# Kernel optimization log

Hardware: AMD Instinct MI355X
Metric: run time of the kernel (lower is better)

The kernel has to match this reference:

```python
import jax, jax.numpy as jnp
import numpy as np

N = 1024
H = 256
EH = max(16, H // 2)  # edge_hidden


def _lin(key, fan_in, fan_out):
    kw, kb = jax.random.split(key)
    s = 1.0 / np.sqrt(fan_in)
    W = jax.random.uniform(kw, (fan_in, fan_out), jnp.float32, -s, s)
    b = jax.random.uniform(kb, (fan_out,), jnp.float32, -s, s)
    return W, b


def setup_inputs() -> dict:
    key = jax.random.key(0)
    ks = jax.random.split(key, 14)
    inp = {
        'h': jax.random.normal(ks[0], (N, H), jnp.float32),
        'delta_local': jax.random.normal(ks[1], (N, 3), jnp.float32),
        't_emb': jax.random.normal(ks[2], (N, 3), jnp.float32),
        'x_current': jax.random.normal(ks[3], (N, 3), jnp.float32),
        'frames': jax.random.normal(ks[4], (N, 3, 3), jnp.float32),
    }
    inp['np1_w'], inp['np1_b'] = _lin(ks[5], H + 6, H)
    inp['np2_w'], inp['np2_b'] = _lin(ks[6], H, H)
    inp['src_w'], inp['src_b'] = _lin(ks[7], H, 1)
    inp['dst_w'], inp['dst_b'] = _lin(ks[8], H, 1)
    inp['ns_w'], inp['ns_b'] = _lin(ks[9], H, 1)
    inp['eg1_w'], inp['eg1_b'] = _lin(ks[10], 4, EH)
    inp['eg2_w'], inp['eg2_b'] = _lin(ks[11], EH, 1)
    inp['out1_w'], inp['out1_b'] = _lin(ks[12], H + 6, H)
    inp['out2_w'], inp['out2_b'] = _lin(ks[13], H, 3)
    return inp


def reference(h, delta_local, t_emb, x_current, frames,
              np1_w, np1_b, np2_w, np2_b,
              src_w, src_b, dst_w, dst_b, ns_w, ns_b,
              eg1_w, eg1_b, eg2_w, eg2_b,
              out1_w, out1_b, out2_w, out2_b):
    silu = jax.nn.silu
    # node_proj: two Linear+SiLU on [h, delta_local, t_emb]
    node_feat = jnp.concatenate([h, delta_local, t_emb], axis=-1)  # [N, H+6]
    node_hidden = silu(silu(node_feat @ np1_w + np1_b) @ np2_w + np2_b)  # [N, H]

    # relative positions in each node's local frame
    rel = x_current[None, :, :] - x_current[:, None, :]             # [N, N, 3], rel[n,m]=x[m]-x[n]
    rel_local = jnp.einsum('nji,nmj->nmi', frames, rel)             # frames^T @ rel
    dist = jnp.linalg.norm(rel_local, axis=-1, keepdims=True)       # [N, N, 1]
    edge_feat = jnp.concatenate([rel_local, dist], axis=-1)         # [N, N, 4]

    # edge-gated attention logits: src + dst + per-edge MLP score
    src = (node_hidden @ src_w + src_b)                             # [N, 1]
    dst = (node_hidden @ dst_w + dst_b)                             # [N, 1]
    edge_logit = silu(edge_feat @ eg1_w + eg1_b) @ eg2_w + eg2_b    # [N, N, 1]
    logits = src[:, None, 0] + dst[None, :, 0] + edge_logit[..., 0] # [N, N]

    eye = jnp.eye(N, dtype=bool)
    logits = jnp.where(eye, -10000.0, logits)
    attn = jax.nn.softmax(logits, axis=1)
    attn = jnp.where(eye, 0.0, attn)
    attn = attn / jnp.maximum(attn.sum(axis=1, keepdims=True), 1e-6)

    ns = jax.nn.sigmoid(node_hidden @ ns_w + ns_b)[:, 0]            # [N]
    local_messages = jnp.einsum('nm,m,nmi->ni', attn, ns, rel_local)  # [N, 3]

    update_feat = jnp.concatenate([node_hidden, delta_local, local_messages], axis=-1)
    local_update = silu(update_feat @ out1_w + out1_b) @ out2_w + out2_b  # [N, 3]
    return local_update + 0.25 * local_messages
```

## Files before the change

kernel.cpp:

```cpp
#include <hip/hip_runtime.h>

#define N 1024
#define H 256
#define EH 128

__device__ __forceinline__ float fast_silu(float x) {
    float u = __builtin_amdgcn_exp2f(x * -1.44269504088896340736f);
    return x * __builtin_amdgcn_rcpf(1.0f + u);
}

__global__ __launch_bounds__(256) void k_node(
    const float* __restrict__ h, const float* __restrict__ dl, const float* __restrict__ temb,
    const float* __restrict__ np1_w, const float* __restrict__ np1_b,
    const float* __restrict__ np2_w, const float* __restrict__ np2_b,
    const float* __restrict__ src_w, const float* __restrict__ src_b,
    const float* __restrict__ dst_w, const float* __restrict__ dst_b,
    const float* __restrict__ ns_w, const float* __restrict__ ns_b,
    const float* __restrict__ eg1_w, const float* __restrict__ eg1_b,
    const float* __restrict__ eg2_w,
    float* __restrict__ nh, float* __restrict__ srcv, float* __restrict__ dstv,
    float* __restrict__ nsv, float* __restrict__ wpA, float* __restrict__ wpB)
{
    const int TILE = 4;
    __shared__ float feat[TILE][264];
    __shared__ float red[TILE][3][4];
    const int tid = threadIdx.x;
    const int blk = blockIdx.x;
    const int n0 = blk * TILE;

    if (blk == 0 && tid < EH) {
        const float NL2E = -1.44269504088896340736f;
        const float NLN2 = -0.69314718055994530942f;
        float4 a;
        a.x = NL2E * eg1_w[0 * EH + tid];
        a.y = NL2E * eg1_w[1 * EH + tid];
        a.z = NL2E * eg1_w[2 * EH + tid];
        a.w = NL2E * eg1_w[3 * EH + tid];
        ((float4*)wpA)[tid] = a;
        float2 b;
        b.x = NL2E * eg1_b[tid];
        b.y = NLN2 * eg2_w[tid];
        ((float2*)wpB)[tid] = b;
    }

    for (int idx = tid; idx < TILE * 264; idx += 256) {
        int t = idx / 264, i = idx % 264;
        int n = n0 + t;
        float v = 0.0f;
        if (i < H)            v = h[n * H + i];
        else if (i < H + 3)   v = dl[n * 3 + (i - H)];
        else if (i < H + 6)   v = temb[n * 3 + (i - H - 3)];
        feat[t][i] = v;
    }
    __syncthreads();

    const int j = tid;
    float acc[TILE];
#pragma unroll
    for (int t = 0; t < TILE; t++) acc[t] = np1_b[j];
    int i = 0;
    for (; i + 4 <= 262; i += 4) {
        float w0 = np1_w[(i + 0) * H + j];
        float w1 = np1_w[(i + 1) * H + j];
        float w2 = np1_w[(i + 2) * H + j];
        float w3 = np1_w[(i + 3) * H + j];
#pragma unroll
        for (int t = 0; t < TILE; t++) {
            float4 f = *(const float4*)&feat[t][i];
            acc[t] = fmaf(f.x, w0, fmaf(f.y, w1, fmaf(f.z, w2, fmaf(f.w, w3, acc[t]))));
        }
    }
    for (; i < 262; i++) {
        float w = np1_w[i * H + j];
#pragma unroll
        for (int t = 0; t < TILE; t++) acc[t] = fmaf(feat[t][i], w, acc[t]);
    }
    __syncthreads();
#pragma unroll
    for (int t = 0; t < TILE; t++) feat[t][j] = fast_silu(acc[t]);
    __syncthreads();

#pragma unroll
    for (int t = 0; t < TILE; t++) acc[t] = np2_b[j];
    for (int i2 = 0; i2 < H; i2 += 4) {
        float w0 = np2_w[(i2 + 0) * H + j];
        float w1 = np2_w[(i2 + 1) * H + j];
        float w2 = np2_w[(i2 + 2) * H + j];
        float w3 = np2_w[(i2 + 3) * H + j];
#pragma unroll
        for (int t = 0; t < TILE; t++) {
            float4 f = *(const float4*)&feat[t][i2];
            acc[t] = fmaf(f.x, w0, fmaf(f.y, w1, fmaf(f.z, w2, fmaf(f.w, w3, acc[t]))));
        }
    }
    float hj[TILE];
#pragma unroll
    for (int t = 0; t < TILE; t++) {
        hj[t] = fast_silu(acc[t]);
        nh[(n0 + t) * H + j] = hj[t];
    }

    float wsc = src_w[j], wdc = dst_w[j], wnc = ns_w[j];
    const int lane = tid & 63, wv = tid >> 6;
#pragma unroll
    for (int t = 0; t < TILE; t++) {
        float ps = hj[t] * wsc, pd = hj[t] * wdc, pn = hj[t] * wnc;
#pragma unroll
        for (int o = 32; o > 0; o >>= 1) {
            ps += __shfl_down(ps, o);
            pd += __shfl_down(pd, o);
            pn += __shfl_down(pn, o);
        }
        if (lane == 0) { red[t][0][wv] = ps; red[t][1][wv] = pd; red[t][2][wv] = pn; }
    }
    __syncthreads();
    if (tid < TILE) {
        int t = tid;
        float s  = red[t][0][0] + red[t][0][1] + red[t][0][2] + red[t][0][3] + src_b[0];
        float d  = red[t][1][0] + red[t][1][1] + red[t][1][2] + red[t][1][3] + dst_b[0];
        float nl = red[t][2][0] + red[t][2][1] + red[t][2][2] + red[t][2][3] + ns_b[0];
        srcv[n0 + t] = s;
        dstv[n0 + t] = d;
        nsv[n0 + t]  = __builtin_amdgcn_rcpf(1.0f + __builtin_amdgcn_exp2f(nl * -1.44269504088896340736f));
    }
}

__global__ __launch_bounds__(256) void k_edge(
    const float* __restrict__ x, const float* __restrict__ frames,
    const float* __restrict__ srcv, const float* __restrict__ dstv,
    const float* __restrict__ nsv,
    const float* __restrict__ wpA, const float* __restrict__ wpB,
    const float* __restrict__ eg2_b, float* __restrict__ msg)
{
    __shared__ float4 WA[EH];
    __shared__ float2 WB[EH];
    __shared__ float rmax[4];
    __shared__ float rsum[4];
    __shared__ float rmsg[3][4];
    const int tid = threadIdx.x;
    const int n = blockIdx.x;

    if (tid < EH) {
        WA[tid] = ((const float4*)wpA)[tid];
        WB[tid] = ((const float2*)wpB)[tid];
    }

    float F[9];
#pragma unroll
    for (int q = 0; q < 9; q++) F[q] = frames[n * 9 + q];
    const float xn0 = x[n * 3 + 0], xn1 = x[n * 3 + 1], xn2 = x[n * 3 + 2];
    const float src_n = srcv[n];
    const float eg2b = eg2_b[0];
    __syncthreads();

    float rl[4][3], dist[4], dstm[4], nsm[4];
#pragma unroll
    for (int e = 0; e < 4; e++) {
        int m = tid + e * 256;
        float rx = x[m * 3 + 0] - xn0;
        float ry = x[m * 3 + 1] - xn1;
        float rz = x[m * 3 + 2] - xn2;
        float r0 = F[0] * rx + F[3] * ry + F[6] * rz;
        float r1 = F[1] * rx + F[4] * ry + F[7] * rz;
        float r2 = F[2] * rx + F[5] * ry + F[8] * rz;
        rl[e][0] = r0; rl[e][1] = r1; rl[e][2] = r2;
        dist[e] = sqrtf(r0 * r0 + r1 * r1 + r2 * r2);
        dstm[e] = dstv[m];
        nsm[e]  = nsv[m];
    }

    float acc[4] = {0.f, 0.f, 0.f, 0.f};
#pragma unroll 4
    for (int k = 0; k < EH; k++) {
        float4 w = WA[k];
        float2 c = WB[k];
#pragma unroll
        for (int e = 0; e < 4; e++) {
            float t2 = fmaf(rl[e][0], w.x, fmaf(rl[e][1], w.y, fmaf(rl[e][2], w.z, fmaf(dist[e], w.w, c.x))));
            float r = __builtin_amdgcn_rcpf(1.0f + __builtin_amdgcn_exp2f(t2));
            acc[e] = fmaf(t2 * r, c.y, acc[e]);
        }
    }

    float lg[4];
#pragma unroll
    for (int e = 0; e < 4; e++) {
        int m = tid + e * 256;
        lg[e] = (m == n) ? -10000.0f : (src_n + dstm[e] + acc[e] + eg2b);
    }

    const int lane = tid & 63, wv = tid >> 6;
    float mx = fmaxf(fmaxf(lg[0], lg[1]), fmaxf(lg[2], lg[3]));
#pragma unroll
    for (int o = 32; o > 0; o >>= 1) mx = fmaxf(mx, __shfl_down(mx, o));
    if (lane == 0) rmax[wv] = mx;
    __syncthreads();
    mx = fmaxf(fmaxf(rmax[0], rmax[1]), fmaxf(rmax[2], rmax[3]));

    float p[4]; float s = 0.f;
#pragma unroll
    for (int e = 0; e < 4; e++) {
        p[e] = __builtin_amdgcn_exp2f((lg[e] - mx) * 1.44269504088896340736f);
        s += p[e];
    }
#pragma unroll
    for (int o = 32; o > 0; o >>= 1) s += __shfl_down(s, o);
    if (lane == 0) rsum[wv] = s;
    __syncthreads();
    float S = rsum[0] + rsum[1] + rsum[2] + rsum[3];
    float inv = 1.0f / S;

    float a0 = 0.f, a1 = 0.f, a2 = 0.f;
#pragma unroll
    for (int e = 0; e < 4; e++) {
        float w = p[e] * inv * nsm[e];
        a0 = fmaf(w, rl[e][0], a0);
        a1 = fmaf(w, rl[e][1], a1);
        a2 = fmaf(w, rl[e][2], a2);
    }
#pragma unroll
    for (int o = 32; o > 0; o >>= 1) {
        a0 += __shfl_down(a0, o);
        a1 += __shfl_down(a1, o);
        a2 += __shfl_down(a2, o);
    }
    if (lane == 0) { rmsg[0][wv] = a0; rmsg[1][wv] = a1; rmsg[2][wv] = a2; }
    __syncthreads();
    if (tid < 3) {
        msg[n * 3 + tid] = rmsg[tid][0] + rmsg[tid][1] + rmsg[tid][2] + rmsg[tid][3];
    }
}

__global__ __launch_bounds__(256) void k_out(
    const float* __restrict__ nh, const float* __restrict__ dl, const float* __restrict__ msg,
    const float* __restrict__ out1_w, const float* __restrict__ out1_b,
    const float* __restrict__ out2_w, const float* __restrict__ out2_b,
    float* __restrict__ out)
{
    const int TILE = 4;
    __shared__ float feat[TILE][264];
    __shared__ float red[TILE][3][4];
    const int tid = threadIdx.x;
    const int blk = blockIdx.x;
    const int n0 = blk * TILE;

    for (int idx = tid; idx < TILE * 264; idx += 256) {
        int t = idx / 264, i = idx % 264;
        int n = n0 + t;
        float v = 0.0f;
        if (i < H)          v = nh[n * H + i];
        else if (i < H + 3) v = dl[n * 3 + (i - H)];
        else if (i < H + 6) v = msg[n * 3 + (i - H - 3)];
        feat[t][i] = v;
    }
    __syncthreads();

    const int j = tid;
    float acc[TILE];
#pragma unroll
    for (int t = 0; t < TILE; t++) acc[t] = out1_b[j];
    int i = 0;
    for (; i + 4 <= 262; i += 4) {
        float w0 = out1_w[(i + 0) * H + j];
        float w1 = out1_w[(i + 1) * H + j];
        float w2 = out1_w[(i + 2) * H + j];
        float w3 = out1_w[(i + 3) * H + j];
#pragma unroll
        for (int t = 0; t < TILE; t++) {
            float4 f = *(const float4*)&feat[t][i];
            acc[t] = fmaf(f.x, w0, fmaf(f.y, w1, fmaf(f.z, w2, fmaf(f.w, w3, acc[t]))));
        }
    }
    for (; i < 262; i++) {
        float w = out1_w[i * H + j];
#pragma unroll
        for (int t = 0; t < TILE; t++) acc[t] = fmaf(feat[t][i], w, acc[t]);
    }

    float hj[TILE];
#pragma unroll
    for (int t = 0; t < TILE; t++) hj[t] = fast_silu(acc[t]);

    float w0 = out2_w[j * 3 + 0], w1 = out2_w[j * 3 + 1], w2 = out2_w[j * 3 + 2];
    const int lane = tid & 63, wv = tid >> 6;
#pragma unroll
    for (int t = 0; t < TILE; t++) {
        float p0 = hj[t] * w0, p1 = hj[t] * w1, p2 = hj[t] * w2;
#pragma unroll
        for (int o = 32; o > 0; o >>= 1) {
            p0 += __shfl_down(p0, o);
            p1 += __shfl_down(p1, o);
            p2 += __shfl_down(p2, o);
        }
        if (lane == 0) { red[t][0][wv] = p0; red[t][1][wv] = p1; red[t][2][wv] = p2; }
    }
    __syncthreads();
    if (tid < TILE * 3) {
        int t = tid / 3, d = tid % 3;
        float v = red[t][d][0] + red[t][d][1] + red[t][d][2] + red[t][d][3] + out2_b[d];
        int n = n0 + t;
        out[n * 3 + d] = v + 0.25f * msg[n * 3 + d];
    }
}

extern "C" void kernel_launch(void* const* d_in, const int* in_sizes, int n_in,
                              void* d_out, int out_size, void* d_ws, size_t ws_size,
                              hipStream_t stream) {
    const float* h      = (const float*)d_in[0];
    const float* dl     = (const float*)d_in[1];
    const float* temb   = (const float*)d_in[2];
    const float* x      = (const float*)d_in[3];
    const float* fr     = (const float*)d_in[4];
    const float* np1_w  = (const float*)d_in[5];
    const float* np1_b  = (const float*)d_in[6];
    const float* np2_w  = (const float*)d_in[7];
    const float* np2_b  = (const float*)d_in[8];
    const float* src_w  = (const float*)d_in[9];
    const float* src_b  = (const float*)d_in[10];
    const float* dst_w  = (const float*)d_in[11];
    const float* dst_b  = (const float*)d_in[12];
    const float* ns_w   = (const float*)d_in[13];
    const float* ns_b   = (const float*)d_in[14];
    const float* eg1_w  = (const float*)d_in[15];
    const float* eg1_b  = (const float*)d_in[16];
    const float* eg2_w  = (const float*)d_in[17];
    const float* eg2_b  = (const float*)d_in[18];
    const float* out1_w = (const float*)d_in[19];
    const float* out1_b = (const float*)d_in[20];
    const float* out2_w = (const float*)d_in[21];
    const float* out2_b = (const float*)d_in[22];

    float* ws   = (float*)d_ws;
    float* nh   = ws;
    float* srcv = nh + 1024 * 256;
    float* dstv = srcv + 1024;
    float* nsv  = dstv + 1024;
    float* msg  = nsv + 1024;
    float* wpA  = msg + 1024 * 3;
    float* wpB  = wpA + 512;

    k_node<<<256, 256, 0, stream>>>(h, dl, temb, np1_w, np1_b, np2_w, np2_b,
                                    src_w, src_b, dst_w, dst_b, ns_w, ns_b,
                                    eg1_w, eg1_b, eg2_w,
                                    nh, srcv, dstv, nsv, wpA, wpB);
    k_edge<<<1024, 256, 0, stream>>>(x, fr, srcv, dstv, nsv, wpA, wpB, eg2_b, msg);
    k_out<<<256, 256, 0, stream>>>(nh, dl, msg, out1_w, out1_b, out2_w, out2_b, (float*)d_out);
}
```

Baseline: 174.7 us.

## Split MLP reduction dimension across 4 thread segments and widen edge blocks

The node and output MLP kernels now launch 1024 threads per block and split each matmul's input dimension into four segments, combining the partial sums through shared memory. This is meant to raise parallelism and latency hiding for the small-row GEMVs. The edge kernel moves to 512 threads with 2 edges per thread instead of 4, giving more waves per block at the cost of wider cross-wave reductions. Extra shared-memory reductions and barriers are added in exchange.

```diff
diff --git a/kernel.cpp b/kernel.cpp
--- a/kernel.cpp
+++ b/kernel.cpp
@@ -9,7 +9,7 @@
     return x * __builtin_amdgcn_rcpf(1.0f + u);
 }
 
-__global__ __launch_bounds__(256) void k_node(
+__global__ __launch_bounds__(1024) void k_node(
     const float* __restrict__ h, const float* __restrict__ dl, const float* __restrict__ temb,
     const float* __restrict__ np1_w, const float* __restrict__ np1_b,
     const float* __restrict__ np2_w, const float* __restrict__ np2_b,
@@ -21,14 +21,15 @@
     float* __restrict__ nh, float* __restrict__ srcv, float* __restrict__ dstv,
     float* __restrict__ nsv, float* __restrict__ wpA, float* __restrict__ wpB)
 {
-    const int TILE = 4;
-    __shared__ float feat[TILE][264];
-    __shared__ float red[TILE][3][4];
+    __shared__ float feat[4][264];
+    __shared__ float sred[4][4][256];
+    __shared__ float gred[4][3][4];
     const int tid = threadIdx.x;
-    const int blk = blockIdx.x;
-    const int n0 = blk * TILE;
-
-    if (blk == 0 && tid < EH) {
+    const int j   = tid & 255;
+    const int seg = tid >> 8;
+    const int n0  = blockIdx.x * 4;
+
+    if (blockIdx.x == 0 && tid < EH) {
         const float NL2E = -1.44269504088896340736f;
         const float NLN2 = -0.69314718055994530942f;
         float4 a;
@@ -43,7 +44,7 @@
         ((float2*)wpB)[tid] = b;
     }
 
-    for (int idx = tid; idx < TILE * 264; idx += 256) {
+    for (int idx = tid; idx < 4 * 264; idx += 1024) {
         int t = idx / 264, i = idx % 264;
         int n = n0 + t;
         float v = 0.0f;
@@ -54,78 +55,84 @@
     }
     __syncthreads();
 
-    const int j = tid;
-    float acc[TILE];
-#pragma unroll
-    for (int t = 0; t < TILE; t++) acc[t] = np1_b[j];
-    int i = 0;
-    for (; i + 4 <= 262; i += 4) {
-        float w0 = np1_w[(i + 0) * H + j];
-        float w1 = np1_w[(i + 1) * H + j];
-        float w2 = np1_w[(i + 2) * H + j];
-        float w3 = np1_w[(i + 3) * H + j];
-#pragma unroll
-        for (int t = 0; t < TILE; t++) {
-            float4 f = *(const float4*)&feat[t][i];
-            acc[t] = fmaf(f.x, w0, fmaf(f.y, w1, fmaf(f.z, w2, fmaf(f.w, w3, acc[t]))));
-        }
-    }
-    for (; i < 262; i++) {
-        float w = np1_w[i * H + j];
-#pragma unroll
-        for (int t = 0; t < TILE; t++) acc[t] = fmaf(feat[t][i], w, acc[t]);
-    }
-    __syncthreads();
-#pragma unroll
-    for (int t = 0; t < TILE; t++) feat[t][j] = fast_silu(acc[t]);
-    __syncthreads();
-
-#pragma unroll
-    for (int t = 0; t < TILE; t++) acc[t] = np2_b[j];
-    for (int i2 = 0; i2 < H; i2 += 4) {
-        float w0 = np2_w[(i2 + 0) * H + j];
-        float w1 = np2_w[(i2 + 1) * H + j];
-        float w2 = np2_w[(i2 + 2) * H + j];
-        float w3 = np2_w[(i2 + 3) * H + j];
-#pragma unroll
-        for (int t = 0; t < TILE; t++) {
-            float4 f = *(const float4*)&feat[t][i2];
-            acc[t] = fmaf(f.x, w0, fmaf(f.y, w1, fmaf(f.z, w2, fmaf(f.w, w3, acc[t]))));
-        }
-    }
-    float hj[TILE];
-#pragma unroll
-    for (int t = 0; t < TILE; t++) {
-        hj[t] = fast_silu(acc[t]);
-        nh[(n0 + t) * H + j] = hj[t];
-    }
-
-    float wsc = src_w[j], wdc = dst_w[j], wnc = ns_w[j];
-    const int lane = tid & 63, wv = tid >> 6;
-#pragma unroll
-    for (int t = 0; t < TILE; t++) {
-        float ps = hj[t] * wsc, pd = hj[t] * wdc, pn = hj[t] * wnc;
+    {
+        float a0 = 0.f, a1 = 0.f, a2 = 0.f, a3 = 0.f;
+        const int lo = seg * 66;
+        const int hi = lo + ((seg == 3) ? 64 : 66);
+        for (int i = lo; i < hi; i += 2) {
+            float w0 = np1_w[i * H + j];
+            float w1 = np1_w[(i + 1) * H + j];
+            float2 f0 = *(const float2*)&feat[0][i];
+            float2 f1 = *(const float2*)&feat[1][i];
+            float2 f2 = *(const float2*)&feat[2][i];
+            float2 f3 = *(const float2*)&feat[3][i];
+            a0 = fmaf(f0.x, w0, fmaf(f0.y, w1, a0));
+            a1 = fmaf(f1.x, w0, fmaf(f1.y, w1, a1));
+            a2 = fmaf(f2.x, w0, fmaf(f2.y, w1, a2));
+            a3 = fmaf(f3.x, w0, fmaf(f3.y, w1, a3));
+        }
+        sred[0][seg][j] = a0;
+        sred[1][seg][j] = a1;
+        sred[2][seg][j] = a2;
+        sred[3][seg][j] = a3;
+    }
+    __syncthreads();
+    {
+        float s = sred[seg][0][j] + sred[seg][1][j] + sred[seg][2][j] + sred[seg][3][j] + np1_b[j];
+        float hv = fast_silu(s);
+        feat[seg][j] = hv;
+    }
+    __syncthreads();
+
+    {
+        float a0 = 0.f, a1 = 0.f, a2 = 0.f, a3 = 0.f;
+        const int lo = seg * 64;
+        for (int i = lo; i < lo + 64; i += 2) {
+            float w0 = np2_w[i * H + j];
+            float w1 = np2_w[(i + 1) * H + j];
+            float2 f0 = *(const float2*)&feat[0][i];
+            float2 f1 = *(const float2*)&feat[1][i];
+            float2 f2 = *(const float2*)&feat[2][i];
+            float2 f3 = *(const float2*)&feat[3][i];
+            a0 = fmaf(f0.x, w0, fmaf(f0.y, w1, a0));
+            a1 = fmaf(f1.x, w0, fmaf(f1.y, w1, a1));
+            a2 = fmaf(f2.x, w0, fmaf(f2.y, w1, a2));
+            a3 = fmaf(f3.x, w0, fmaf(f3.y, w1, a3));
+        }
+        sred[0][seg][j] = a0;
+        sred[1][seg][j] = a1;
+        sred[2][seg][j] = a2;
+        sred[3][seg][j] = a3;
+    }
+    __syncthreads();
+
+    float h2 = fast_silu(sred[seg][0][j] + sred[seg][1][j] + sred[seg][2][j] + sred[seg][3][j] + np2_b[j]);
+    nh[(n0 + seg) * H + j] = h2;
+
+    {
+        float ps = h2 * src_w[j], pd = h2 * dst_w[j], pn = h2 * ns_w[j];
+        const int lane = tid & 63, wvl = (tid >> 6) & 3;
 #pragma unroll
         for (int o = 32; o > 0; o >>= 1) {
             ps += __shfl_down(ps, o);
             pd += __shfl_down(pd, o);
             pn += __shfl_down(pn, o);
         }
-        if (lane == 0) { red[t][0][wv] = ps; red[t][1][wv] = pd; red[t][2][wv] = pn; }
-    }
-    __syncthreads();
-    if (tid < TILE) {
+        if (lane == 0) { gred[seg][0][wvl] = ps; gred[seg][1][wvl] = pd; gred[seg][2][wvl] = pn; }
+    }
+    __syncthreads();
+    if (tid < 4) {
         int t = tid;
-        float s  = red[t][0][0] + red[t][0][1] + red[t][0][2] + red[t][0][3] + src_b[0];
-        float d  = red[t][1][0] + red[t][1][1] + red[t][1][2] + red[t][1][3] + dst_b[0];
-        float nl = red[t][2][0] + red[t][2][1] + red[t][2][2] + red[t][2][3] + ns_b[0];
+        float s  = gred[t][0][0] + gred[t][0][1] + gred[t][0][2] + gred[t][0][3] + src_b[0];
+        float d  = gred[t][1][0] + gred[t][1][1] + gred[t][1][2] + gred[t][1][3] + dst_b[0];
+        float nl = gred[t][2][0] + gred[t][2][1] + gred[t][2][2] + gred[t][2][3] + ns_b[0];
         srcv[n0 + t] = s;
         dstv[n0 + t] = d;
         nsv[n0 + t]  = __builtin_amdgcn_rcpf(1.0f + __builtin_amdgcn_exp2f(nl * -1.44269504088896340736f));
     }
 }
 
-__global__ __launch_bounds__(256) void k_edge(
+__global__ __launch_bounds__(512) void k_edge(
     const float* __restrict__ x, const float* __restrict__ frames,
     const float* __restrict__ srcv, const float* __restrict__ dstv,
     const float* __restrict__ nsv,
@@ -134,9 +141,9 @@
 {
     __shared__ float4 WA[EH];
     __shared__ float2 WB[EH];
-    __shared__ float rmax[4];
-    __shared__ float rsum[4];
-    __shared__ float rmsg[3][4];
+    __shared__ float rmax[8];
+    __shared__ float rsum[8];
+    __shared__ float rmsg[3][8];
     const int tid = threadIdx.x;
     const int n = blockIdx.x;
 
@@ -153,10 +160,10 @@
     const float eg2b = eg2_b[0];
     __syncthreads();
 
-    float rl[4][3], dist[4], dstm[4], nsm[4];
-#pragma unroll
-    for (int e = 0; e < 4; e++) {
-        int m = tid + e * 256;
+    float rl[2][3], dist[2], dstm[2], nsm[2];
+#pragma unroll
+    for (int e = 0; e < 2; e++) {
+        int m = tid + e * 512;
         float rx = x[m * 3 + 0] - xn0;
         float ry = x[m * 3 + 1] - xn1;
         float rz = x[m * 3 + 2] - xn2;
@@ -169,37 +176,39 @@
         nsm[e]  = nsv[m];
     }
 
-    float acc[4] = {0.f, 0.f, 0.f, 0.f};
+    float acc[2] = {0.f, 0.f};
 #pragma unroll 4
     for (int k = 0; k < EH; k++) {
         float4 w = WA[k];
         float2 c = WB[k];
 #pragma unroll
-        for (int e = 0; e < 4; e++) {
+        for (int e = 0; e < 2; e++) {
             float t2 = fmaf(rl[e][0], w.x, fmaf(rl[e][1], w.y, fmaf(rl[e][2], w.z, fmaf(dist[e], w.w, c.x))));
             float r = __builtin_amdgcn_rcpf(1.0f + __builtin_amdgcn_exp2f(t2));
             acc[e] = fmaf(t2 * r, c.y, acc[e]);
         }
     }
 
-    float lg[4];
-#pragma unroll
-    for (int e = 0; e < 4; e++) {
-        int m = tid + e * 256;
+    float lg[2];
+#pragma unroll
+    for (int e = 0; e < 2; e++) {
+        int m = tid + e * 512;
         lg[e] = (m == n) ? -10000.0f : (src_n + dstm[e] + acc[e] + eg2b);
     }
 
     const int lane = tid & 63, wv = tid >> 6;
-    float mx = fmaxf(fmaxf(lg[0], lg[1]), fmaxf(lg[2], lg[3]));
+    float mx = fmaxf(lg[0], lg[1]);
 #pragma unroll
     for (int o = 32; o > 0; o >>= 1) mx = fmaxf(mx, __shfl_down(mx, o));
     if (lane == 0) rmax[wv] = mx;
     __syncthreads();
-    mx = fmaxf(fmaxf(rmax[0], rmax[1]), fmaxf(rmax[2], rmax[3]));
-
-    float p[4]; float s = 0.f;
-#pragma unroll
-    for (int e = 0; e < 4; e++) {
+    mx = rmax[0];
+#pragma unroll
+    for (int q = 1; q < 8; q++) mx = fmaxf(mx, rmax[q]);
+
+    float p[2]; float s = 0.f;
+#pragma unroll
+    for (int e = 0; e < 2; e++) {
         p[e] = __builtin_amdgcn_exp2f((lg[e] - mx) * 1.44269504088896340736f);
         s += p[e];
     }
@@ -207,12 +216,12 @@
     for (int o = 32; o > 0; o >>= 1) s += __shfl_down(s, o);
     if (lane == 0) rsum[wv] = s;
     __syncthreads();
-    float S = rsum[0] + rsum[1] + rsum[2] + rsum[3];
+    float S = rsum[0] + rsum[1] + rsum[2] + rsum[3] + rsum[4] + rsum[5] + rsum[6] + rsum[7];
     float inv = 1.0f / S;
 
     float a0 = 0.f, a1 = 0.f, a2 = 0.f;
 #pragma unroll
-    for (int e = 0; e < 4; e++) {
+    for (int e = 0; e < 2; e++) {
         float w = p[e] * inv * nsm[e];
         a0 = fmaf(w, rl[e][0], a0);
         a1 = fmaf(w, rl[e][1], a1);
@@ -227,24 +236,28 @@
     if (lane == 0) { rmsg[0][wv] = a0; rmsg[1][wv] = a1; rmsg[2][wv] = a2; }
     __syncthreads();
     if (tid < 3) {
-        msg[n * 3 + tid] = rmsg[tid][0] + rmsg[tid][1] + rmsg[tid][2] + rmsg[tid][3];
-    }
-}
-
-__global__ __launch_bounds__(256) void k_out(
+        float v = 0.f;
+#pragma unroll
+        for (int q = 0; q < 8; q++) v += rmsg[tid][q];
+        msg[n * 3 + tid] = v;
+    }
+}
+
+__global__ __launch_bounds__(1024) void k_out(
     const float* __restrict__ nh, const float* __restrict__ dl, const float* __restrict__ msg,
     const float* __restrict__ out1_w, const float* __restrict__ out1_b,
     const float* __restrict__ out2_w, const float* __restrict__ out2_b,
     float* __restrict__ out)
 {
-    const int TILE = 4;
-    __shared__ float feat[TILE][264];
-    __shared__ float red[TILE][3][4];
+    __shared__ float feat[4][264];
+    __shared__ float sred[4][4][256];
+    __shared__ float gred[4][3][4];
     const int tid = threadIdx.x;
-    const int blk = blockIdx.x;
-    const int n0 = blk * TILE;
-
-    for (int idx = tid; idx < TILE * 264; idx += 256) {
+    const int j   = tid & 255;
+    const int seg = tid >> 8;
+    const int n0  = blockIdx.x * 4;
+
+    for (int idx = tid; idx < 4 * 264; idx += 1024) {
         int t = idx / 264, i = idx % 264;
         int n = n0 + t;
         float v = 0.0f;
@@ -255,49 +268,46 @@
     }
     __syncthreads();
 
-    const int j = tid;
-    float acc[TILE];
-#pragma unroll
-    for (int t = 0; t < TILE; t++) acc[t] = out1_b[j];
-    int i = 0;
-    for (; i + 4 <= 262; i += 4) {
-        float w0 = out1_w[(i + 0) * H + j];
-        float w1 = out1_w[(i + 1) * H + j];
-        float w2 = out1_w[(i + 2) * H + j];
-        float w3 = out1_w[(i + 3) * H + j];
-#pragma unroll
-        for (int t = 0; t < TILE; t++) {
-            float4 f = *(const float4*)&feat[t][i];
-            acc[t] = fmaf(f.x, w0, fmaf(f.y, w1, fmaf(f.z, w2, fmaf(f.w, w3, acc[t]))));
-        }
-    }
-    for (; i < 262; i++) {
-        float w = out1_w[i * H + j];
-#pragma unroll
-        for (int t = 0; t < TILE; t++) acc[t] = fmaf(feat[t][i], w, acc[t]);
-    }
-
-    float hj[TILE];
-#pragma unroll
-    for (int t = 0; t < TILE; t++) hj[t] = fast_silu(acc[t]);
-
-    float w0 = out2_w[j * 3 + 0], w1 = out2_w[j * 3 + 1], w2 = out2_w[j * 3 + 2];
-    const int lane = tid & 63, wv = tid >> 6;
-#pragma unroll
-    for (int t = 0; t < TILE; t++) {
-        float p0 = hj[t] * w0, p1 = hj[t] * w1, p2 = hj[t] * w2;
+    {
+        float a0 = 0.f, a1 = 0.f, a2 = 0.f, a3 = 0.f;
+        const int lo = seg * 66;
+        const int hi = lo + ((seg == 3) ? 64 : 66);
+        for (int i = lo; i < hi; i += 2) {
+            float w0 = out1_w[i * H + j];
+            float w1 = out1_w[(i + 1) * H + j];
+            float2 f0 = *(const float2*)&feat[0][i];
+            float2 f1 = *(const float2*)&feat[1][i];
+            float2 f2 = *(const float2*)&feat[2][i];
+            float2 f3 = *(const float2*)&feat[3][i];
+            a0 = fmaf(f0.x, w0, fmaf(f0.y, w1, a0));
+            a1 = fmaf(f1.x, w0, fmaf(f1.y, w1, a1));
+            a2 = fmaf(f2.x, w0, fmaf(f2.y, w1, a2));
+            a3 = fmaf(f3.x, w0, fmaf(f3.y, w1, a3));
+        }
+        sred[0][seg][j] = a0;
+        sred[1][seg][j] = a1;
+        sred[2][seg][j] = a2;
+        sred[3][seg][j] = a3;
+    }
+    __syncthreads();
+
+    float hv = fast_silu(sred[seg][0][j] + sred[seg][1][j] + sred[seg][2][j] + sred[seg][3][j] + out1_b[j]);
+    {
+        float w0 = out2_w[j * 3 + 0], w1 = out2_w[j * 3 + 1], w2 = out2_w[j * 3 + 2];
+        float p0 = hv * w0, p1 = hv * w1, p2 = hv * w2;
+        const int lane = tid & 63, wvl = (tid >> 6) & 3;
 #pragma unroll
         for (int o = 32; o > 0; o >>= 1) {
             p0 += __shfl_down(p0, o);
             p1 += __shfl_down(p1, o);
             p2 += __shfl_down(p2, o);
         }
-        if (lane == 0) { red[t][0][wv] = p0; red[t][1][wv] = p1; red[t][2][wv] = p2; }
-    }
-    __syncthreads();
-    if (tid < TILE * 3) {
+        if (lane == 0) { gred[seg][0][wvl] = p0; gred[seg][1][wvl] = p1; gred[seg][2][wvl] = p2; }
+    }
+    __syncthreads();
+    if (tid < 12) {
         int t = tid / 3, d = tid % 3;
-        float v = red[t][d][0] + red[t][d][1] + red[t][d][2] + red[t][d][3] + out2_b[d];
+        float v = gred[t][d][0] + gred[t][d][1] + gred[t][d][2] + gred[t][d][3] + out2_b[d];
         int n = n0 + t;
         out[n * 3 + d] = v + 0.25f * msg[n * 3 + d];
     }
@@ -339,10 +349,10 @@
     float* wpA  = msg + 1024 * 3;
     float* wpB  = wpA + 512;
 
-    k_node<<<256, 256, 0, stream>>>(h, dl, temb, np1_w, np1_b, np2_w, np2_b,
-                                    src_w, src_b, dst_w, dst_b, ns_w, ns_b,
-                                    eg1_w, eg1_b, eg2_w,
-                                    nh, srcv, dstv, nsv, wpA, wpB);
-    k_edge<<<1024, 256, 0, stream>>>(x, fr, srcv, dstv, nsv, wpA, wpB, eg2_b, msg);
-    k_out<<<256, 256, 0, stream>>>(nh, dl, msg, out1_w, out1_b, out2_w, out2_b, (float*)d_out);
-}
+    k_node<<<256, 1024, 0, stream>>>(h, dl, temb, np1_w, np1_b, np2_w, np2_b,
+                                     src_w, src_b, dst_w, dst_b, ns_w, ns_b,
+                                     eg1_w, eg1_b, eg2_w,
+                                     nh, srcv, dstv, nsv, wpA, wpB);
+    k_edge<<<1024, 512, 0, stream>>>(x, fr, srcv, dstv, nsv, wpA, wpB, eg2_b, msg);
+    k_out<<<256, 1024, 0, stream>>>(nh, dl, msg, out1_w, out1_b, out2_w, out2_b, (float*)d_out);
+}
```

New measurement: 161.6 us. 7.5% less time.
